# Performance work log

Measured on AMD Instinct MI355X. Metric: run time of the kernel, lower is better.

## Reference

```python
import jax, jax.numpy as jnp
import numpy as np
from jax import lax

LATTICE = (16, 16)          # translation-group shape
N_CELLS = 16 * 16           # 256
N_POINT = 8                 # point-group size (e.g. square-lattice C4v)
N_SYMM = N_POINT * N_CELLS  # 2048
FEATURES = 64
IN_FEATURES = 64
BATCH = 64


def setup_inputs() -> dict:
    key = jax.random.key(0)
    k1, k2, k3, k4 = jax.random.split(key, 4)
    x = jax.random.normal(k1, (BATCH, IN_FEATURES, N_SYMM), dtype=jnp.float32)
    kernel = jax.random.normal(k2, (FEATURES, IN_FEATURES, N_SYMM), dtype=jnp.float32) * (
        1.0 / np.sqrt(IN_FEATURES * N_SYMM)
    )
    bias = jax.random.normal(k3, (FEATURES,), dtype=jnp.float32) * 0.02
    product_table = jax.random.randint(k4, (N_POINT, N_SYMM), 0, N_SYMM, dtype=jnp.int64)
    return {"x": x, "kernel": kernel, "bias": bias, "product_table": product_table}


def reference(x, kernel, bias, product_table):
    batch_shape = x.shape[:-2]
    in_features = x.shape[-2]
    # mapping: pt[:n_point] -> (n_point, n_point, *lattice)
    mapping = (
        product_table.reshape(N_POINT, N_CELLS, N_POINT)
        .transpose(0, 2, 1)
        .reshape(N_POINT, N_POINT, *LATTICE)
    )
    # activations: (..., in_f, n_symm) -> (B, in_f, n_point, *lattice)
    xg = x.reshape(-1, in_features, N_CELLS, N_POINT).transpose(0, 1, 3, 2)
    xg = xg.reshape(*xg.shape[:-1], *LATTICE)
    # equivariant kernel via gather: (feat, in_f, n_point, n_point, *lattice)
    kg = kernel[..., mapping]
    # FFT over the translation lattice
    xf = jnp.fft.fftn(xg, s=LATTICE).reshape(*xg.shape[:3], N_CELLS)       # (B,in_f,np,cells)
    kf = jnp.fft.fftn(kg, s=LATTICE).reshape(*kg.shape[:4], N_CELLS)       # (F,in_f,np,np,cells)
    # batched complex contraction over (in_f, n_point), batch over cells
    y = lax.dot_general(xf, kf, (((1, 2), (1, 2)), ((3,), (4,))))          # (cells,B,F,np)
    y = y.transpose(1, 2, 3, 0)                                            # (B,F,np,cells)
    y = y.reshape(*y.shape[:3], *LATTICE)
    y = jnp.fft.ifftn(y, s=LATTICE).reshape(*y.shape[:3], N_CELLS)
    y = y.transpose(0, 1, 3, 2).reshape(*batch_shape, FEATURES, N_SYMM)
    y = y + bias[:, None]
    # input dtype is float32 -> complex result cannot cast back, return real part
    return y.real.astype(jnp.float32)
```

## Files before the change

kernel.cpp:

```cpp
#include <hip/hip_runtime.h>

typedef __attribute__((ext_vector_type(8))) short bf16x8;
typedef __attribute__((ext_vector_type(16))) float f32x16;
typedef unsigned short ushort_t;

constexpr int NS  = 2048;
constexpr int F   = 64;
constexpr int IFT = 64;
constexpr int B   = 64;
constexpr int NCS = 144;

constexpr float CT[16] = {
    1.0f,  0.9238795325112867f,  0.7071067811865476f,  0.3826834323650898f,
    0.0f, -0.3826834323650898f, -0.7071067811865476f, -0.9238795325112867f,
   -1.0f, -0.9238795325112867f, -0.7071067811865476f, -0.3826834323650898f,
    0.0f,  0.3826834323650898f,  0.7071067811865476f,  0.9238795325112867f};
constexpr float ST[16] = {
    0.0f,  0.3826834323650898f,  0.7071067811865476f,  0.9238795325112867f,
    1.0f,  0.9238795325112867f,  0.7071067811865476f,  0.3826834323650898f,
    0.0f, -0.3826834323650898f, -0.7071067811865476f, -0.9238795325112867f,
   -1.0f, -0.9238795325112867f, -0.7071067811865476f, -0.3826834323650898f};

constexpr int DR4[16] = {0,4,8,12, 1,5,9,13, 2,6,10,14, 3,7,11,15};

template<bool INV>
__device__ inline void dft4(float& ar, float& ai, float& br, float& bi,
                            float& cr, float& ci, float& dr, float& di)
{
    const float t0r = ar + cr, t0i = ai + ci;
    const float t1r = ar - cr, t1i = ai - ci;
    const float t2r = br + dr, t2i = bi + di;
    const float t3r = br - dr, t3i = bi - di;
    ar = t0r + t2r; ai = t0i + t2i;
    cr = t0r - t2r; ci = t0i - t2i;
    if (!INV) { br = t1r + t3i; bi = t1i - t3r; dr = t1r - t3i; di = t1i + t3r; }
    else      { br = t1r - t3i; bi = t1i + t3r; dr = t1r + t3i; di = t1i - t3r; }
}

template<bool INV>
__device__ inline void fft16(float* xr, float* xi)
{
#pragma unroll
    for (int r = 0; r < 4; ++r)
        dft4<INV>(xr[r], xi[r], xr[r + 4], xi[r + 4],
                  xr[r + 8], xi[r + 8], xr[r + 12], xi[r + 12]);
#pragma unroll
    for (int r = 1; r < 4; ++r)
#pragma unroll
        for (int q = 1; q < 4; ++q) {
            const int t = (r * q) & 15;
            const int s = r + 4 * q;
            if (t == 4) {
                const float tr = xr[s];
                if (!INV) { xr[s] = xi[s];  xi[s] = -tr; }
                else      { xr[s] = -xi[s]; xi[s] = tr;  }
            } else {
                const float c = CT[t], sn = INV ? ST[t] : -ST[t];
                const float tr = xr[s];
                xr[s] = tr * c - xi[s] * sn;
                xi[s] = tr * sn + xi[s] * c;
            }
        }
#pragma unroll
    for (int q = 0; q < 4; ++q)
        dft4<INV>(xr[4 * q], xi[4 * q], xr[4 * q + 1], xi[4 * q + 1],
                  xr[4 * q + 2], xi[4 * q + 2], xr[4 * q + 3], xi[4 * q + 3]);
}

__device__ inline ushort_t f2bf(float x) {
    unsigned u = __float_as_uint(x);
    unsigned r = u + 0x7FFFu + ((u >> 16) & 1u);
    return (ushort_t)(r >> 16);
}
__device__ inline float bf2f(ushort_t h) { return __uint_as_float(((unsigned)h) << 16); }

__device__ inline bf16x8 bneg(bf16x8 v) {
    union { bf16x8 b; unsigned u[4]; } x; x.b = v;
    x.u[0] ^= 0x80008000u; x.u[1] ^= 0x80008000u;
    x.u[2] ^= 0x80008000u; x.u[3] ^= 0x80008000u;
    return x.b;
}

__global__ __launch_bounds__(256) void permute_pt_kernel(
    const int* __restrict__ pt, int* __restrict__ pt2)
{
    const int t = blockIdx.x * 256 + threadIdx.x;
    const int a = t >> 11, r = t & 2047;
    const int bq = r >> 8, s = r & 255;
    pt2[t] = pt[a * NS + s * 8 + bq];
}

__global__ __launch_bounds__(256, 4) void fft_x_kernel(
    const float* __restrict__ x, ushort_t* __restrict__ xf, int i0, int KB)
{
    __shared__ float t_re[16][152], t_im[16][152];
    __shared__ ushort_t stgx[NCS * 68];
    const int tid = threadIdx.x;
    const int bp = blockIdx.x;
    const int il = blockIdx.y;

    const int g = tid >> 4, l = tid & 15;
    const int bloc = g & 1, a = g >> 1;
    const int b = bp * 2 + bloc;
    const int i = i0 + il;

    const float* xr_g = x + ((size_t)b * IFT + i) * NS;
    float xr[16], xi[16];
#pragma unroll
    for (int sx = 0; sx < 16; ++sx) { xr[sx] = xr_g[(l * 16 + sx) * 8 + a]; xi[sx] = 0.f; }
    fft16<false>(xr, xi);
#pragma unroll
    for (int kx = 0; kx < 9; ++kx) {
        t_re[g][kx * 17 + l] = xr[DR4[kx]];
        t_im[g][kx * 17 + l] = xi[DR4[kx]];
    }
    __syncthreads();

    if (l < 9) {
        float Tr[16], Ti[16];
#pragma unroll
        for (int n = 0; n < 16; ++n) { Tr[n] = t_re[g][l * 17 + n]; Ti[n] = t_im[g][l * 17 + n]; }
        fft16<false>(Tr, Ti);
#pragma unroll
        for (int ky = 0; ky < 16; ++ky) {
            const float sr = Tr[DR4[ky]], si = Ti[DR4[ky]];
            const int cs = ky * 9 + l;
            const ushort_t rh = f2bf(sr); const ushort_t rl = f2bf(sr - bf2f(rh));
            const ushort_t ih = f2bf(si); const ushort_t ilo = f2bf(si - bf2f(ih));
            const unsigned w0 = (unsigned)rh | ((unsigned)rl << 16);
            const unsigned w1 = (unsigned)ih | ((unsigned)ilo << 16);
            *(uint2*)&stgx[cs * 68 + bloc * 32 + a * 4] = make_uint2(w0, w1);
        }
    }
    __syncthreads();

    const int kb = il >> 1, mt = bp >> 4;
    const int lb = (il & 1) * 32 + (bp & 15) * 2;
    for (int t = tid; t < NCS * 8; t += 256) {
        const int cs = t >> 3, v4 = (t >> 1) & 3, h = t & 1;
        union { ushort_t s[8]; uint4 u; } tmp;
        const int base = cs * 68 + h * 32 + (v4 >> 1) * 2 + (v4 & 1);
#pragma unroll
        for (int j = 0; j < 8; ++j) tmp.s[j] = stgx[base + j * 4];
        const size_t off = ((((size_t)cs * KB + kb) * 2 + mt) * 4 + v4) * 512 + (size_t)(lb + h) * 8;
        *(uint4*)(xf + off) = tmp.u;
    }
}

__global__ __launch_bounds__(256, 4) void fft_k_kernel(
    const float* __restrict__ kern, const int* __restrict__ pt2,
    ushort_t* __restrict__ kf, int i0, int KB)
{
    __shared__ float krow[2048];
    __shared__ float t_re[16][152], t_im[16][152];
    __shared__ unsigned stgk[NCS * 18];
    const int tid = threadIdx.x;
    const int bx = blockIdx.x;
    const int il = blockIdx.y;
    const int fg = bx >> 2, bqp = bx & 3;
    const int i = i0 + il;

    const int g = tid >> 4, l = tid & 15;
    const int bql = g & 1, a = g >> 1;
    const int bq = bqp * 2 + bql;

    int idx[16];
    const int4* pp = (const int4*)(pt2 + ((a * 8 + bq) * 256 + l * 16));
#pragma unroll
    for (int q = 0; q < 4; ++q) {
        const int4 t4 = pp[q];
        idx[q * 4] = t4.x; idx[q * 4 + 1] = t4.y; idx[q * 4 + 2] = t4.z; idx[q * 4 + 3] = t4.w;
    }

    const int kb = il >> 1;
    for (int fr = 0; fr < 4; ++fr) {
        const int f = fg * 4 + fr;
        __syncthreads();
        {
            const float4* src = (const float4*)(kern + ((size_t)f * IFT + i) * NS);
            for (int u = tid; u < 512; u += 256) ((float4*)krow)[u] = src[u];
        }
        __syncthreads();

        float xr[16], xi[16];
#pragma unroll
        for (int sx = 0; sx < 16; ++sx) { xr[sx] = krow[idx[sx]]; xi[sx] = 0.f; }
        fft16<false>(xr, xi);
#pragma unroll
        for (int kx = 0; kx < 9; ++kx) {
            t_re[g][kx * 17 + l] = xr[DR4[kx]];
            t_im[g][kx * 17 + l] = xi[DR4[kx]];
        }
        __syncthreads();

        if (l < 9) {
            float Tr[16], Ti[16];
#pragma unroll
            for (int n = 0; n < 16; ++n) { Tr[n] = t_re[g][l * 17 + n]; Ti[n] = t_im[g][l * 17 + n]; }
            fft16<false>(Tr, Ti);
#pragma unroll
            for (int ky = 0; ky < 16; ++ky) {
                const int cs = ky * 9 + l;
                stgk[cs * 18 + bql * 8 + a] =
                    (unsigned)f2bf(Tr[DR4[ky]]) | ((unsigned)f2bf(Ti[DR4[ky]]) << 16);
            }
        }
        __syncthreads();

        const int nt = f >> 2;
        const int lbase = (il & 1) * 32 + (f & 3) * 8 + bqp * 2;
        for (int t = tid; t < NCS * 2; t += 256) {
            const int cs = t >> 1, h = t & 1;
            const int base = cs * 18 + h * 8;
            unsigned w[8];
            *(uint2*)&w[0] = *(const uint2*)&stgk[base];
            *(uint2*)&w[2] = *(const uint2*)&stgk[base + 2];
            *(uint2*)&w[4] = *(const uint2*)&stgk[base + 4];
            *(uint2*)&w[6] = *(const uint2*)&stgk[base + 6];
            union { ushort_t s[8]; uint4 u; } lo, hi;
#pragma unroll
            for (int j = 0; j < 8; ++j) { lo.s[j] = (ushort_t)(w[j] & 0xffffu); hi.s[j] = (ushort_t)(w[j] >> 16); }
            const size_t off0 = ((((size_t)cs * KB + kb) * 16 + nt) * 2 + 0) * 512 + (size_t)(lbase + h) * 8;
            *(uint4*)(kf + off0) = lo.u;
            *(uint4*)(kf + off0 + 512) = hi.u;
        }
    }
}

#define MFMA(acc, A, Bv) acc = __builtin_amdgcn_mfma_f32_32x32x16_bf16(A, Bv, acc, 0, 0, 0)
#define LDB(p) (*(const bf16x8*)(p))

__global__ __launch_bounds__(256) void gemm_kernel(
    const ushort_t* __restrict__ xf, const ushort_t* __restrict__ kf,
    float* __restrict__ yre, float* __restrict__ yim, int KB, int acc)
{
    const int cs = blockIdx.y, nb = blockIdx.x;
    const int w = threadIdx.x >> 6, lane = threadIdx.x & 63;
    const int nt = nb * 4 + w;

    f32x16 cre0, cim0, cre1, cim1;
#pragma unroll
    for (int q = 0; q < 16; ++q) { cre0[q] = 0.f; cim0[q] = 0.f; cre1[q] = 0.f; cim1[q] = 0.f; }

    const ushort_t* ab = xf + (size_t)cs * KB * 4096 + (size_t)lane * 8;
    const ushort_t* bb = kf + (size_t)cs * KB * 16384 + (size_t)nt * 1024 + (size_t)lane * 8;

    bf16x8 Brh = LDB(bb), Bih = LDB(bb + 512);
    bf16x8 Arh0 = LDB(ab), Arl0 = LDB(ab + 512), Aih0 = LDB(ab + 1024), Ail0 = LDB(ab + 1536);
    bf16x8 Arh1 = LDB(ab + 2048), Arl1 = LDB(ab + 2560), Aih1 = LDB(ab + 3072), Ail1 = LDB(ab + 3584);

    for (int kb = 0; kb < KB; ++kb) {
        const int kn = (kb + 1 < KB) ? kb + 1 : kb;
        const ushort_t* an = ab + (size_t)kn * 4096;
        const ushort_t* bn = bb + (size_t)kn * 16384;
        const bf16x8 nBrh = LDB(bn), nBih = LDB(bn + 512);
        const bf16x8 nArh0 = LDB(an), nArl0 = LDB(an + 512), nAih0 = LDB(an + 1024), nAil0 = LDB(an + 1536);
        const bf16x8 nArh1 = LDB(an + 2048), nArl1 = LDB(an + 2560), nAih1 = LDB(an + 3072), nAil1 = LDB(an + 3584);

        const bf16x8 NAih0 = bneg(Aih0), NAil0 = bneg(Ail0);
        const bf16x8 NAih1 = bneg(Aih1), NAil1 = bneg(Ail1);

        MFMA(cre0, Arh0, Brh); MFMA(cre0, Arl0, Brh);
        MFMA(cre0, NAih0, Bih); MFMA(cre0, NAil0, Bih);
        MFMA(cim0, Arh0, Bih); MFMA(cim0, Arl0, Bih);
        MFMA(cim0, Aih0, Brh); MFMA(cim0, Ail0, Brh);
        MFMA(cre1, Arh1, Brh); MFMA(cre1, Arl1, Brh);
        MFMA(cre1, NAih1, Bih); MFMA(cre1, NAil1, Bih);
        MFMA(cim1, Arh1, Bih); MFMA(cim1, Arl1, Bih);
        MFMA(cim1, Aih1, Brh); MFMA(cim1, Ail1, Brh);

        Brh = nBrh; Bih = nBih;
        Arh0 = nArh0; Arl0 = nArl0; Aih0 = nAih0; Ail0 = nAil0;
        Arh1 = nArh1; Arl1 = nArl1; Aih1 = nAih1; Ail1 = nAil1;
    }

    const int col = lane & 31, rhi = (lane >> 5) * 4;
    const int n = nb * 128 + w * 32 + col;
#pragma unroll
    for (int mt = 0; mt < 2; ++mt) {
        const f32x16 cr = mt ? cre1 : cre0;
        const f32x16 ci = mt ? cim1 : cim0;
#pragma unroll
        for (int reg = 0; reg < 16; ++reg) {
            const int row = (reg & 3) + 8 * (reg >> 2) + rhi;
            const size_t off = ((size_t)cs * B + mt * 32 + row) * 512 + n;
            float vr = cr[reg], vi = ci[reg];
            if (acc) { vr += yre[off]; vi += yim[off]; }
            yre[off] = vr; yim[off] = vi;
        }
    }
}

__global__ __launch_bounds__(256, 4) void ifft_y_kernel(
    const float* __restrict__ yre, const float* __restrict__ yim,
    const float* __restrict__ bias, float* __restrict__ out)
{
    __shared__ float yr_s[NCS][17], yi_s[NCS][17];
    __shared__ float t_re[16][271], t_im[16][271];
    __shared__ float ost[2][256][9];
    const int tid = threadIdx.x;
    const int ng = blockIdx.x;
    const int b = blockIdx.y;
    const int n0 = ng * 16;
    for (int t = tid; t < NCS * 16; t += 256) {
        const int cs = t >> 4, nl = t & 15;
        const size_t off = ((size_t)cs * B + b) * 512 + n0 + nl;
        yr_s[cs][nl] = yre[off];
        yi_s[cs][nl] = yim[off];
    }
    __syncthreads();

    const int g = tid >> 4, l = tid & 15;

    float Yr[16], Yi[16];
#pragma unroll
    for (int kx = 0; kx < 16; ++kx) {
        if (kx <= 8) {
            const int cs = l * 9 + kx;
            Yr[kx] = yr_s[cs][g]; Yi[kx] = yi_s[cs][g];
        } else {
            const int cs = ((16 - l) & 15) * 9 + (16 - kx);
            Yr[kx] = yr_s[cs][g]; Yi[kx] = -yi_s[cs][g];
        }
    }
    fft16<true>(Yr, Yi);
#pragma unroll
    for (int sx = 0; sx < 16; ++sx) {
        t_re[g][sx * 17 + l] = Yr[DR4[sx]];
        t_im[g][sx * 17 + l] = Yi[DR4[sx]];
    }
    __syncthreads();

    float Tr[16], Ti[16];
#pragma unroll
    for (int n = 0; n < 16; ++n) { Tr[n] = t_re[g][l * 17 + n]; Ti[n] = t_im[g][l * 17 + n]; }
    fft16<true>(Tr, Ti);
    const int fl = g >> 3, pq = g & 7;
#pragma unroll
    for (int sy = 0; sy < 16; ++sy)
        ost[fl][sy * 16 + l][pq] = Tr[DR4[sy]] * (1.f / 256.f);
    __syncthreads();

    const int f0 = ng * 2;
    for (int t = tid; t < 4096; t += 256) {
        const int flv = t >> 11, e = t & 2047;
        out[((size_t)b * F + f0 + flv) * NS + e] = ost[flv][e >> 3][e & 7] + bias[f0 + flv];
    }
}

extern "C" void kernel_launch(void* const* d_in, const int* in_sizes, int n_in,
                              void* d_out, int out_size, void* d_ws, size_t ws_size,
                              hipStream_t stream)
{
    const float* x = (const float*)d_in[0];
    const float* kern = (const float*)d_in[1];
    const float* bias = (const float*)d_in[2];
    const int* pt = (const int*)d_in[3];
    float* out = (float*)d_out;

    int CI = 2;
    const int cands[6] = {64, 32, 16, 8, 4, 2};
    for (int t = 0; t < 6; ++t) {
        const int KBc = cands[t] / 2;
        const size_t need = 65536
                          + (size_t)NCS * KBc * 8192
                          + (size_t)NCS * KBc * 32768
                          + 2 * (size_t)NCS * B * 512 * 4;
        if (need <= ws_size) { CI = cands[t]; break; }
    }
    const int KB = CI / 2;

    char* p = (char*)d_ws;
    int* pt2 = (int*)p;          p += 65536;
    ushort_t* xf = (ushort_t*)p; p += (size_t)NCS * KB * 8192;
    ushort_t* kf = (ushort_t*)p; p += (size_t)NCS * KB * 32768;
    float* yre = (float*)p;      p += (size_t)NCS * B * 512 * 4;
    float* yim = (float*)p;

    permute_pt_kernel<<<64, 256, 0, stream>>>(pt, pt2);

    const int nch = IFT / CI;
    for (int ch = 0; ch < nch; ++ch) {
        const int i0 = ch * CI;
        fft_x_kernel<<<dim3(32, CI), 256, 0, stream>>>(x, xf, i0, KB);
        fft_k_kernel<<<dim3(64, CI), 256, 0, stream>>>(kern, pt2, kf, i0, KB);
        gemm_kernel<<<dim3(4, NCS), 256, 0, stream>>>(xf, kf, yre, yim, KB, ch > 0);
    }
    ifft_y_kernel<<<dim3(32, B), 256, 0, stream>>>(yre, yim, bias, out);
}
```

Before: 326.4 us.

## Reorganize spectral buffers plane-major and batch two kernel rows per FFT pass

Changes the layout of the transformed activations and kernel from cell-major blocks to plane-major, with each real/imag/hi/lo plane strided by the full cell count. The GEMM grid is swapped so adjacent blocks cover adjacent cells. The kernel FFT now loads two feature rows at once, interleaved as float2, and reuses the gather indices for both. It also spreads the second-pass FFT across 144 contiguous threads instead of 9 of every 16, and aliases shared buffers to cut LDS use. Together these aim to make global stores and loads more coalesced and to reduce gather and occupancy costs, at the price of more synchronization per sub-iteration.

```diff
diff --git a/kernel.cpp b/kernel.cpp
--- a/kernel.cpp
+++ b/kernel.cpp
@@ -136,13 +136,14 @@
 
     const int kb = il >> 1, mt = bp >> 4;
     const int lb = (il & 1) * 32 + (bp & 15) * 2;
+    const size_t PS = (size_t)NCS * 512;
     for (int t = tid; t < NCS * 8; t += 256) {
         const int cs = t >> 3, v4 = (t >> 1) & 3, h = t & 1;
         union { ushort_t s[8]; uint4 u; } tmp;
-        const int base = cs * 68 + h * 32 + (v4 >> 1) * 2 + (v4 & 1);
+        const int base = cs * 68 + h * 32 + v4;
 #pragma unroll
         for (int j = 0; j < 8; ++j) tmp.s[j] = stgx[base + j * 4];
-        const size_t off = ((((size_t)cs * KB + kb) * 2 + mt) * 4 + v4) * 512 + (size_t)(lb + h) * 8;
+        const size_t off = (size_t)(kb * 8 + mt * 4 + v4) * PS + (size_t)cs * 512 + (size_t)(lb + h) * 8;
         *(uint4*)(xf + off) = tmp.u;
     }
 }
@@ -151,18 +152,20 @@
     const float* __restrict__ kern, const int* __restrict__ pt2,
     ushort_t* __restrict__ kf, int i0, int KB)
 {
-    __shared__ float krow[2048];
-    __shared__ float t_re[16][152], t_im[16][152];
-    __shared__ unsigned stgk[NCS * 18];
+    __shared__ __align__(16) unsigned uni[4096];
+    __shared__ __align__(16) float2 t2[16 * 153];
+    float2* krow2 = reinterpret_cast<float2*>(uni);
+    unsigned* stgk = uni;
+
     const int tid = threadIdx.x;
-    const int bx = blockIdx.x;
-    const int il = blockIdx.y;
-    const int fg = bx >> 2, bqp = bx & 3;
-    const int i = i0 + il;
+    const int fg  = blockIdx.x & 15;
+    const int bqp = blockIdx.x >> 4;
+    const int il  = blockIdx.y;
+    const int i   = i0 + il;
 
     const int g = tid >> 4, l = tid & 15;
     const int bql = g & 1, a = g >> 1;
-    const int bq = bqp * 2 + bql;
+    const int bq  = bqp * 2 + bql;
 
     int idx[16];
     const int4* pp = (const int4*)(pt2 + ((a * 8 + bq) * 256 + l * 16));
@@ -173,56 +176,77 @@
     }
 
     const int kb = il >> 1;
-    for (int fr = 0; fr < 4; ++fr) {
-        const int f = fg * 4 + fr;
+    const int nt = fg;
+    const int pg = (tid * 57) >> 9;
+    const int pl = tid - pg * 9;
+    const int slot = (pg & 1) * 8 + (pg >> 1);
+    const size_t PS = (size_t)NCS * 512;
+
+    for (int fr2 = 0; fr2 < 2; ++fr2) {
+        const int f0 = fg * 4 + fr2 * 2;
         __syncthreads();
         {
-            const float4* src = (const float4*)(kern + ((size_t)f * IFT + i) * NS);
-            for (int u = tid; u < 512; u += 256) ((float4*)krow)[u] = src[u];
+            const float4* s0 = (const float4*)(kern + ((size_t)f0 * IFT + i) * NS);
+            const float4* s1 = (const float4*)(kern + ((size_t)(f0 + 1) * IFT + i) * NS);
+            for (int u = tid; u < 512; u += 256) {
+                const float4 va = s0[u], vb = s1[u];
+                float4* dst = (float4*)(krow2 + (size_t)u * 4);
+                dst[0] = make_float4(va.x, vb.x, va.y, vb.y);
+                dst[1] = make_float4(va.z, vb.z, va.w, vb.w);
+            }
         }
         __syncthreads();
-
-        float xr[16], xi[16];
-#pragma unroll
-        for (int sx = 0; sx < 16; ++sx) { xr[sx] = krow[idx[sx]]; xi[sx] = 0.f; }
-        fft16<false>(xr, xi);
-#pragma unroll
-        for (int kx = 0; kx < 9; ++kx) {
-            t_re[g][kx * 17 + l] = xr[DR4[kx]];
-            t_im[g][kx * 17 + l] = xi[DR4[kx]];
-        }
-        __syncthreads();
-
-        if (l < 9) {
-            float Tr[16], Ti[16];
-#pragma unroll
-            for (int n = 0; n < 16; ++n) { Tr[n] = t_re[g][l * 17 + n]; Ti[n] = t_im[g][l * 17 + n]; }
-            fft16<false>(Tr, Ti);
-#pragma unroll
-            for (int ky = 0; ky < 16; ++ky) {
-                const int cs = ky * 9 + l;
-                stgk[cs * 18 + bql * 8 + a] =
-                    (unsigned)f2bf(Tr[DR4[ky]]) | ((unsigned)f2bf(Ti[DR4[ky]]) << 16);
+        float2 v2[16];
+#pragma unroll
+        for (int sx = 0; sx < 16; ++sx) v2[sx] = krow2[idx[sx]];
+
+        for (int sub = 0; sub < 2; ++sub) {
+            {
+                float xr[16], xi[16];
+#pragma unroll
+                for (int sx = 0; sx < 16; ++sx) { xr[sx] = sub ? v2[sx].y : v2[sx].x; xi[sx] = 0.f; }
+                fft16<false>(xr, xi);
+#pragma unroll
+                for (int kx = 0; kx < 9; ++kx)
+                    t2[g * 153 + kx * 17 + l] = make_float2(xr[DR4[kx]], xi[DR4[kx]]);
             }
-        }
-        __syncthreads();
-
-        const int nt = f >> 2;
-        const int lbase = (il & 1) * 32 + (f & 3) * 8 + bqp * 2;
-        for (int t = tid; t < NCS * 2; t += 256) {
-            const int cs = t >> 1, h = t & 1;
-            const int base = cs * 18 + h * 8;
-            unsigned w[8];
-            *(uint2*)&w[0] = *(const uint2*)&stgk[base];
-            *(uint2*)&w[2] = *(const uint2*)&stgk[base + 2];
-            *(uint2*)&w[4] = *(const uint2*)&stgk[base + 4];
-            *(uint2*)&w[6] = *(const uint2*)&stgk[base + 6];
-            union { ushort_t s[8]; uint4 u; } lo, hi;
-#pragma unroll
-            for (int j = 0; j < 8; ++j) { lo.s[j] = (ushort_t)(w[j] & 0xffffu); hi.s[j] = (ushort_t)(w[j] >> 16); }
-            const size_t off0 = ((((size_t)cs * KB + kb) * 16 + nt) * 2 + 0) * 512 + (size_t)(lbase + h) * 8;
-            *(uint4*)(kf + off0) = lo.u;
-            *(uint4*)(kf + off0 + 512) = hi.u;
+            __syncthreads();
+
+            if (tid < 144) {
+                float Tr[16], Ti[16];
+#pragma unroll
+                for (int n = 0; n < 16; ++n) {
+                    const float2 tv = t2[pg * 153 + pl * 17 + n];
+                    Tr[n] = tv.x; Ti[n] = tv.y;
+                }
+                fft16<false>(Tr, Ti);
+#pragma unroll
+                for (int ky = 0; ky < 16; ++ky) {
+                    const int cs = ky * 9 + pl;
+                    stgk[cs * 18 + slot] =
+                        (unsigned)f2bf(Tr[DR4[ky]]) | ((unsigned)f2bf(Ti[DR4[ky]]) << 16);
+                }
+            }
+            __syncthreads();
+
+            const int f = f0 + sub;
+            const int lbase = (il & 1) * 32 + (f & 3) * 8 + bqp * 2;
+            for (int t = tid; t < NCS * 2; t += 256) {
+                const int cs = t >> 1, h = t & 1;
+                const int base = cs * 18 + h * 8;
+                unsigned w[8];
+                *(uint2*)&w[0] = *(const uint2*)&stgk[base];
+                *(uint2*)&w[2] = *(const uint2*)&stgk[base + 2];
+                *(uint2*)&w[4] = *(const uint2*)&stgk[base + 4];
+                *(uint2*)&w[6] = *(const uint2*)&stgk[base + 6];
+                union { ushort_t s[8]; uint4 u; } lo, hi;
+#pragma unroll
+                for (int j = 0; j < 8; ++j) { lo.s[j] = (ushort_t)(w[j] & 0xffffu); hi.s[j] = (ushort_t)(w[j] >> 16); }
+                const size_t off = (size_t)(kb * 32 + nt * 2) * PS + (size_t)cs * 512 + (size_t)(lbase + h) * 8;
+                *(uint4*)(kf + off) = lo.u;
+                *(uint4*)(kf + off + PS) = hi.u;
+            }
+            __syncthreads();
         }
     }
 }
@@ -234,28 +258,31 @@
     const ushort_t* __restrict__ xf, const ushort_t* __restrict__ kf,
     float* __restrict__ yre, float* __restrict__ yim, int KB, int acc)
 {
-    const int cs = blockIdx.y, nb = blockIdx.x;
+    const int cs = blockIdx.x, nb = blockIdx.y;
     const int w = threadIdx.x >> 6, lane = threadIdx.x & 63;
     const int nt = nb * 4 + w;
+    const size_t PS = (size_t)NCS * 512;
 
     f32x16 cre0, cim0, cre1, cim1;
 #pragma unroll
     for (int q = 0; q < 16; ++q) { cre0[q] = 0.f; cim0[q] = 0.f; cre1[q] = 0.f; cim1[q] = 0.f; }
 
-    const ushort_t* ab = xf + (size_t)cs * KB * 4096 + (size_t)lane * 8;
-    const ushort_t* bb = kf + (size_t)cs * KB * 16384 + (size_t)nt * 1024 + (size_t)lane * 8;
-
-    bf16x8 Brh = LDB(bb), Bih = LDB(bb + 512);
-    bf16x8 Arh0 = LDB(ab), Arl0 = LDB(ab + 512), Aih0 = LDB(ab + 1024), Ail0 = LDB(ab + 1536);
-    bf16x8 Arh1 = LDB(ab + 2048), Arl1 = LDB(ab + 2560), Aih1 = LDB(ab + 3072), Ail1 = LDB(ab + 3584);
+    const ushort_t* ab = xf + (size_t)cs * 512 + (size_t)lane * 8;
+    const ushort_t* bb = kf + (size_t)cs * 512 + (size_t)(nt * 2) * PS + (size_t)lane * 8;
+
+    const ushort_t* ap = ab;
+    const ushort_t* bp = bb;
+    bf16x8 Brh = LDB(bp), Bih = LDB(bp + PS);
+    bf16x8 Arh0 = LDB(ap), Arl0 = LDB(ap + PS), Aih0 = LDB(ap + 2 * PS), Ail0 = LDB(ap + 3 * PS);
+    bf16x8 Arh1 = LDB(ap + 4 * PS), Arl1 = LDB(ap + 5 * PS), Aih1 = LDB(ap + 6 * PS), Ail1 = LDB(ap + 7 * PS);
 
     for (int kb = 0; kb < KB; ++kb) {
         const int kn = (kb + 1 < KB) ? kb + 1 : kb;
-        const ushort_t* an = ab + (size_t)kn * 4096;
-        const ushort_t* bn = bb + (size_t)kn * 16384;
-        const bf16x8 nBrh = LDB(bn), nBih = LDB(bn + 512);
-        const bf16x8 nArh0 = LDB(an), nArl0 = LDB(an + 512), nAih0 = LDB(an + 1024), nAil0 = LDB(an + 1536);
-        const bf16x8 nArh1 = LDB(an + 2048), nArl1 = LDB(an + 2560), nAih1 = LDB(an + 3072), nAil1 = LDB(an + 3584);
+        const ushort_t* an = ab + (size_t)kn * 8 * PS;
+        const ushort_t* bn = bb + (size_t)kn * 32 * PS;
+        const bf16x8 nBrh = LDB(bn), nBih = LDB(bn + PS);
+        const bf16x8 nArh0 = LDB(an), nArl0 = LDB(an + PS), nAih0 = LDB(an + 2 * PS), nAil0 = LDB(an + 3 * PS);
+        const bf16x8 nArh1 = LDB(an + 4 * PS), nArl1 = LDB(an + 5 * PS), nAih1 = LDB(an + 6 * PS), nAil1 = LDB(an + 7 * PS);
 
         const bf16x8 NAih0 = bneg(Aih0), NAil0 = bneg(Ail0);
         const bf16x8 NAih1 = bneg(Aih1), NAil1 = bneg(Ail1);
@@ -384,7 +411,7 @@
         const int i0 = ch * CI;
         fft_x_kernel<<<dim3(32, CI), 256, 0, stream>>>(x, xf, i0, KB);
         fft_k_kernel<<<dim3(64, CI), 256, 0, stream>>>(kern, pt2, kf, i0, KB);
-        gemm_kernel<<<dim3(4, NCS), 256, 0, stream>>>(xf, kf, yre, yim, KB, ch > 0);
+        gemm_kernel<<<dim3(NCS, 4), 256, 0, stream>>>(xf, kf, yre, yim, KB, ch > 0);
     }
     ifft_y_kernel<<<dim3(32, B), 256, 0, stream>>>(yre, yim, bias, out);
 }
```

New measurement: 290.9 us. 1.12x faster.
